# Performance work log

Measured on AMD Instinct MI355X. Metric: run time of the kernel, lower is better.

## Reference

```python
import jax, jax.numpy as jnp
import numpy as np


def _gcn_norm(edge_index, num_nodes):
    # Add self-loops (PyG SGConv default add_self_loops=True) and compute
    # symmetric normalization deg^-1/2 * A_hat * deg^-1/2.
    src, dst = edge_index[0], edge_index[1]
    loop = jnp.arange(num_nodes, dtype=src.dtype)
    src = jnp.concatenate([src, loop])
    dst = jnp.concatenate([dst, loop])
    ones = jnp.ones(src.shape[0], dtype=jnp.float32)
    deg = jax.ops.segment_sum(ones, dst, num_segments=num_nodes)
    dis = jnp.where(deg > 0, jax.lax.rsqrt(deg), 0.0)
    norm = dis[src] * dis[dst]  # per-edge weight
    return src, dst, norm


def _propagate(h, src, dst, norm, num_nodes, K):
    # K rounds of normalized sparse propagation: h <- A_hat_norm @ h
    for _ in range(K):
        h = jax.ops.segment_sum(h[src] * norm[:, None], dst, num_segments=num_nodes)
    return h


def setup_inputs() -> dict:
    key = jax.random.key(0)
    k1, k2, k3, k4 = jax.random.split(key, 4)
    N, E, F, H, C = 100000, 1600000, 128, 64, 40
    x = jax.random.normal(k1, (N, F), dtype=jnp.float32)
    edge_index = jax.random.randint(k2, (2, E), 0, N, dtype=jnp.int64)
    W1 = jax.random.normal(k3, (F, H), dtype=jnp.float32) * (1.0 / np.sqrt(F))
    b1 = jnp.zeros((H,), dtype=jnp.float32)
    W2 = jax.random.normal(k4, (H, C), dtype=jnp.float32) * (1.0 / np.sqrt(H))
    b2 = jnp.zeros((C,), dtype=jnp.float32)
    return {"x": x, "edge_index": edge_index, "W1": W1, "b1": b1, "W2": W2, "b2": b2}


def reference(x, edge_index, W1, b1, W2, b2):
    N = x.shape[0]
    K = 2
    src, dst, norm = _gcn_norm(edge_index, N)
    # SGConv layer 1: K-hop propagation then linear
    h = _propagate(x, src, dst, norm, N, K)
    h = h @ W1 + b1
    h = jax.nn.relu(h)
    # SGConv layer 2
    h = _propagate(h, src, dst, norm, N, K)
    h = h @ W2 + b2
    return jax.nn.log_softmax(h, axis=1)
```

## Files before the change

kernel.cpp:

```cpp
#include <hip/hip_runtime.h>
#include <hip/hip_fp16.h>
#include <math.h>

__host__ __device__ static inline int div_up(long long a, long long b) { return (int)((a + b - 1) / b); }

#define SCH 2048
#define PM 256
#define BKN 256
#define CAP 8192
#define PROPG 2048

struct h8 { __half2 a, b, c, d; };
struct h4 { __half2 a, b; };

typedef _Float16 half8v __attribute__((ext_vector_type(8)));
typedef float f32x4v __attribute__((ext_vector_type(4)));

__device__ inline int nt_load1(const int* p) {
    return __builtin_nontemporal_load(p);
}
__device__ inline h4 f4toh4(float4 v) {
    h4 o;
    o.a = __float22half2_rn(make_float2(v.x, v.y));
    o.b = __float22half2_rn(make_float2(v.z, v.w));
    return o;
}


__global__ __launch_bounds__(256) void k_histA(const int* __restrict__ dst,
                                               int* __restrict__ histA,
                                               int E, int NBK) {
    __shared__ int h[1024];
    const int tid = threadIdx.x, c = blockIdx.x;
    for (int i = tid; i < NBK; i += 256) h[i] = 0;
    __syncthreads();
    const int ce = (div_up(E, PM) + 3) & ~3;
    const int e0 = c * ce, e1 = min(E, e0 + ce);
    int i = e0 + tid * 4;
    for (; i + 3 < e1; i += 256 * 4) {
        int4 d = *reinterpret_cast<const int4*>(dst + i);
        atomicAdd(&h[d.x >> 8], 1);
        atomicAdd(&h[d.y >> 8], 1);
        atomicAdd(&h[d.z >> 8], 1);
        atomicAdd(&h[d.w >> 8], 1);
    }
    for (int j = i; j < e1; ++j) atomicAdd(&h[dst[j] >> 8], 1);
    __syncthreads();
    for (int b = tid; b < NBK; b += 256) histA[b * PM + c] = h[b];
}

__global__ void k_scan_part(const int* __restrict__ a, int* __restrict__ bsum, int len) {
    __shared__ int ws[4];
    int base = blockIdx.x * SCH + threadIdx.x * 8;
    int t = 0;
#pragma unroll
    for (int j = 0; j < 8; ++j) {
        int idx = base + j;
        if (idx < len) t += a[idx];
    }
    for (int off = 32; off >= 1; off >>= 1) t += __shfl_xor(t, off);
    int lane = threadIdx.x & 63, wid = threadIdx.x >> 6;
    if (lane == 0) ws[wid] = t;
    __syncthreads();
    if (threadIdx.x == 0) bsum[blockIdx.x] = ws[0] + ws[1] + ws[2] + ws[3];
}

__global__ void k_scan_bsums(int* __restrict__ bsum, int* __restrict__ tot, int NB) {
    __shared__ int wsum[16];
    int tid = threadIdx.x;
    int v = (tid < NB) ? bsum[tid] : 0;
    int lane = tid & 63, wid = tid >> 6;
    int x = v;
    for (int off = 1; off < 64; off <<= 1) {
        int y = __shfl_up(x, off);
        if (lane >= off) x += y;
    }
    if (lane == 63) wsum[wid] = x;
    __syncthreads();
    if (tid < 16) {
        int s = wsum[tid];
        for (int off = 1; off < 16; off <<= 1) {
            int y = __shfl_up(s, off);
            if (tid >= off) s += y;
        }
        wsum[tid] = s;
    }
    __syncthreads();
    int woff = (wid > 0) ? wsum[wid - 1] : 0;
    int excl = woff + x - v;
    if (tid < NB) bsum[tid] = excl;
    if (tid == NB - 1) tot[0] = excl + v;
}

__global__ void k_scan_apply(const int* __restrict__ cnt, const int* __restrict__ bsum,
                             int* __restrict__ rp, int* __restrict__ cur,
                             float* __restrict__ dis, float* __restrict__ inv, int N) {
    __shared__ int wsum[4];
    int tid = threadIdx.x;
    int base = blockIdx.x * SCH + tid * 8;
    int v[8];
    int t = 0;
#pragma unroll
    for (int j = 0; j < 8; ++j) {
        int idx = base + j;
        v[j] = (idx < N) ? cnt[idx] : 0;
        t += v[j];
    }
    int lane = tid & 63, wid = tid >> 6;
    int x = t;
    for (int off = 1; off < 64; off <<= 1) {
        int y = __shfl_up(x, off);
        if (lane >= off) x += y;
    }
    if (lane == 63) wsum[wid] = x;
    __syncthreads();
    int woff = 0;
    for (int w = 0; w < wid; ++w) woff += wsum[w];
    int run = bsum[blockIdx.x] + woff + (x - t);
#pragma unroll
    for (int j = 0; j < 8; ++j) {
        int idx = base + j;
        if (idx < N) {
            rp[idx] = run;
            cur[idx] = run;
            float dg = (float)v[j] + 1.0f;
            dis[idx] = rsqrtf(dg);
            inv[idx] = sqrtf(dg);
        }
        run += v[j];
    }
}

__global__ void k_scan_apply_plain(int* __restrict__ a, const int* __restrict__ bsum,
                                   int len) {
    __shared__ int wsum[4];
    int tid = threadIdx.x;
    int base = blockIdx.x * SCH + tid * 8;
    int v[8];
    int t = 0;
#pragma unroll
    for (int j = 0; j < 8; ++j) {
        int idx = base + j;
        v[j] = (idx < len) ? a[idx] : 0;
        t += v[j];
    }
    int lane = tid & 63, wid = tid >> 6;
    int x = t;
    for (int off = 1; off < 64; off <<= 1) {
        int y = __shfl_up(x, off);
        if (lane >= off) x += y;
    }
    if (lane == 63) wsum[wid] = x;
    __syncthreads();
    int woff = 0;
    for (int w = 0; w < wid; ++w) woff += wsum[w];
    int run = bsum[blockIdx.x] + woff + (x - t);
#pragma unroll
    for (int j = 0; j < 8; ++j) {
        int idx = base + j;
        if (idx < len) a[idx] = run;
        run += v[j];
    }
}

__global__ __launch_bounds__(256) void k_partitionA(
        const int* __restrict__ src, const int* __restrict__ dst,
        const int* __restrict__ pbase, unsigned* __restrict__ pairs, int E, int NBK) {
    __shared__ int curb[1024];
    const int tid = threadIdx.x, c = blockIdx.x;
    for (int b = tid; b < NBK; b += 256) curb[b] = pbase[b * PM + c];
    __syncthreads();
    const int ce = (div_up(E, PM) + 3) & ~3;
    const int e0 = c * ce, e1 = min(E, e0 + ce);
    int i = e0 + tid * 4;
    for (; i + 3 < e1; i += 256 * 4) {
        int4 d4 = *reinterpret_cast<const int4*>(dst + i);
        int4 s4 = *reinterpret_cast<const int4*>(src + i);
        int p0 = atomicAdd(&curb[d4.x >> 8], 1); pairs[p0] = ((unsigned)s4.x << 8) | (d4.x & 255);
        int p1 = atomicAdd(&curb[d4.y >> 8], 1); pairs[p1] = ((unsigned)s4.y << 8) | (d4.y & 255);
        int p2 = atomicAdd(&curb[d4.z >> 8], 1); pairs[p2] = ((unsigned)s4.z << 8) | (d4.z & 255);
        int p3 = atomicAdd(&curb[d4.w >> 8], 1); pairs[p3] = ((unsigned)s4.w << 8) | (d4.w & 255);
    }
    for (int j = i; j < e1; ++j) {
        int d = dst[j];
        int p = atomicAdd(&curb[d >> 8], 1);
        pairs[p] = ((unsigned)src[j] << 8) | (d & 255);
    }
}

__global__ __launch_bounds__(256) void k_cntB(
        const unsigned* __restrict__ pairs, const int* __restrict__ pbase,
        int* __restrict__ cnt, int E, int N, int NBK) {
    __shared__ int c256[BKN];
    const int b = blockIdx.x;
    const int tid = threadIdx.x;
    c256[tid] = 0;
    __syncthreads();
    const int base = pbase[b * PM];
    const int end = (b + 1 < NBK) ? pbase[(b + 1) * PM] : E;
    for (int i = base + tid; i < end; i += 256)
        atomicAdd(&c256[pairs[i] & 255], 1);
    __syncthreads();
    int n = b * BKN + tid;
    if (n < N) cnt[n] = c256[tid];
}

__global__ __launch_bounds__(256) void k_placeB(
        const unsigned* __restrict__ pairs, const int* __restrict__ rp,
        int* __restrict__ cur, int* __restrict__ csrc, int N) {
    __shared__ int curl[BKN];
    __shared__ int stage[CAP];
    const int b = blockIdx.x;
    const int n0 = b * BKN;
    const int n1 = min(N, n0 + BKN);
    const int base = rp[n0], end = rp[n1];
    const int cntb = end - base;
    const int tid = threadIdx.x;
    if (cntb <= CAP) {
        if (n0 + tid < n1) curl[tid] = rp[n0 + tid] - base;
        __syncthreads();
        for (int i = base + tid; i < end; i += 256) {
            unsigned pr = pairs[i];
            int p = atomicAdd(&curl[pr & 255], 1);
            stage[p] = (int)(pr >> 8);
        }
        __syncthreads();
        for (int i = tid; i < cntb; i += 256) csrc[base + i] = stage[i];
    } else {
        for (int i = base + tid; i < end; i += 256) {
            unsigned pr = pairs[i];
            int d = n0 + (int)(pr & 255);
            csrc[atomicAdd(&cur[d], 1)] = (int)(pr >> 8);
        }
    }
}


__device__ inline void add_h8(float* acc, const h8& v) {
    float2 f0 = __half22float2(v.a), f1 = __half22float2(v.b);
    float2 f2 = __half22float2(v.c), f3 = __half22float2(v.d);
    acc[0] += f0.x; acc[1] += f0.y;
    acc[2] += f1.x; acc[3] += f1.y;
    acc[4] += f2.x; acc[5] += f2.y;
    acc[6] += f3.x; acc[7] += f3.y;
}

template<int F>
__global__ __launch_bounds__(256) void k_prop_h(
        const int* __restrict__ rp, const int* __restrict__ csrc,
        const float* __restrict__ dis,
        const __half* __restrict__ hin, __half* __restrict__ hout, int N) {
    constexpr int TPE = F / 8;
    const long long total = (long long)N * TPE;
    const long long stride = (long long)gridDim.x * 256;
    for (long long t = (long long)blockIdx.x * 256 + threadIdx.x; t < total; t += stride) {
        int n = (int)(t / TPE);
        int l = (int)(t % TPE);
        float acc[8];
        {
            h8 v = *reinterpret_cast<const h8*>(hin + (size_t)n * F + 8 * l);
#pragma unroll
            for (int j = 0; j < 8; ++j) acc[j] = 0.f;
            add_h8(acc, v);
        }
        int e = rp[n], end = rp[n + 1];
        for (; e + 7 < end; e += 8) {
            int s[8];
            h8 v[8];
#pragma unroll
            for (int j = 0; j < 8; ++j) s[j] = nt_load1(csrc + e + j);
#pragma unroll
            for (int j = 0; j < 8; ++j)
                v[j] = *reinterpret_cast<const h8*>(hin + (size_t)s[j] * F + 8 * l);
#pragma unroll
            for (int j = 0; j < 8; ++j) add_h8(acc, v[j]);
        }
        for (; e < end; ++e) {
            int s = nt_load1(csrc + e);
            h8 v = *reinterpret_cast<const h8*>(hin + (size_t)s * F + 8 * l);
            add_h8(acc, v);
        }
        float dn = dis[n];
        float d2 = dn * dn;
        h8 o;
        o.a = __float22half2_rn(make_float2(acc[0] * d2, acc[1] * d2));
        o.b = __float22half2_rn(make_float2(acc[2] * d2, acc[3] * d2));
        o.c = __float22half2_rn(make_float2(acc[4] * d2, acc[5] * d2));
        o.d = __float22half2_rn(make_float2(acc[6] * d2, acc[7] * d2));
        *reinterpret_cast<h8*>(hout + (size_t)n * F + 8 * l) = o;
    }
}


__global__ __launch_bounds__(256) void k_gemm1(const float* __restrict__ X,
                                               const float* __restrict__ W,
                                               const float* __restrict__ dis,
                                               __half* __restrict__ Y, int N) {
    __shared__ __half sx[64][136];
    const int tid = threadIdx.x;
    const int lane = tid & 63, wv = tid >> 6;
    const int n0 = blockIdx.x * 64;
    const bool full = (n0 + 64 <= N);
    const int krow = (lane >> 4) * 8;
    const int col = lane & 15;

    half8v bfrag[4][4];
#pragma unroll
    for (int ct = 0; ct < 4; ++ct)
#pragma unroll
        for (int ks = 0; ks < 4; ++ks)
#pragma unroll
            for (int j = 0; j < 8; ++j)
                bfrag[ct][ks][j] = (_Float16)W[(ks * 32 + krow + j) * 64 + ct * 16 + col];

    float4 xr[8];
#pragma unroll
    for (int j = 0; j < 8; ++j) {
        int idx = (tid + j * 256) * 4;
        int n = idx >> 7, k = idx & 127;
        float4 v = make_float4(0.f, 0.f, 0.f, 0.f);
        if (full || n0 + n < N)
            v = *reinterpret_cast<const float4*>(X + (size_t)(n0 + n) * 128 + k);
        xr[j] = v;
    }
#pragma unroll
    for (int j = 0; j < 8; ++j) {
        int idx = (tid + j * 256) * 4;
        int n = idx >> 7, k = idx & 127;
        *reinterpret_cast<h4*>(&sx[n][k]) = f4toh4(xr[j]);
    }
    __syncthreads();

    const int m0 = wv * 16;
    f32x4v acc[4] = {{0,0,0,0},{0,0,0,0},{0,0,0,0},{0,0,0,0}};
#pragma unroll
    for (int ks = 0; ks < 4; ++ks) {
        half8v a = *reinterpret_cast<const half8v*>(&sx[m0 + (lane & 15)][ks * 32 + krow]);
#pragma unroll
        for (int ct = 0; ct < 4; ++ct)
            acc[ct] = __builtin_amdgcn_mfma_f32_16x16x32_f16(a, bfrag[ct][ks], acc[ct], 0, 0, 0);
    }

    const int rbase = m0 + (lane >> 4) * 4;
#pragma unroll
    for (int r = 0; r < 4; ++r) {
        int n = n0 + rbase + r;
        if (n < N) {
            float sc = dis[n];
#pragma unroll
            for (int ct = 0; ct < 4; ++ct)
                Y[(size_t)n * 64 + ct * 16 + col] = (__half)(acc[ct][r] * sc);
        }
    }
}

__global__ __launch_bounds__(256) void k_gemm2(const __half* __restrict__ H,
                                               const float* __restrict__ b1,
                                               const float* __restrict__ W2,
                                               const float* __restrict__ dis,
                                               const float* __restrict__ inv,
                                               __half* __restrict__ T, int N) {
    __shared__ float sh[64][68];
    __shared__ float sw[64][68];
    const int tid = threadIdx.x;
    const int n0 = blockIdx.x * 64;
    const bool full = (n0 + 64 <= N);
#pragma unroll
    for (int j = 0; j < 4; ++j) {
        int idx = (tid + j * 256) * 4;
        int k = idx >> 6, h = idx & 63;
        float4 v = make_float4(0.f, 0.f, 0.f, 0.f);
        if (h < 40) v = *reinterpret_cast<const float4*>(W2 + k * 40 + h);
        *reinterpret_cast<float4*>(&sw[k][h]) = v;
    }
#pragma unroll
    for (int j = 0; j < 2; ++j) {
        int idx = (tid + j * 256) * 8;
        int n = idx >> 6, k = idx & 63;
        float v[8];
        if (full || n0 + n < N) {
            float iv = inv[n0 + n];
            h8 hv = *reinterpret_cast<const h8*>(H + (size_t)(n0 + n) * 64 + k);
            float2 f0 = __half22float2(hv.a), f1 = __half22float2(hv.b);
            float2 f2 = __half22float2(hv.c), f3 = __half22float2(hv.d);
            v[0] = f0.x; v[1] = f0.y; v[2] = f1.x; v[3] = f1.y;
            v[4] = f2.x; v[5] = f2.y; v[6] = f3.x; v[7] = f3.y;
#pragma unroll
            for (int q = 0; q < 8; ++q) v[q] = fmaxf(v[q] * iv + b1[k + q], 0.f);
        } else {
#pragma unroll
            for (int q = 0; q < 8; ++q) v[q] = 0.f;
        }
#pragma unroll
        for (int q = 0; q < 8; ++q) sh[n][k + q] = v[q];
    }
    __syncthreads();
    const int lane = tid & 63, wid = tid >> 6;
    const int h0 = (lane & 15) * 4;
    const int nb = wid * 16 + (lane >> 4) * 4;
    float4 a0 = {0,0,0,0}, a1 = {0,0,0,0}, a2 = {0,0,0,0}, a3 = {0,0,0,0};
#define FMA4(a, s, v) { (a).x += (s) * (v).x; (a).y += (s) * (v).y; \
                        (a).z += (s) * (v).z; (a).w += (s) * (v).w; }
#pragma unroll 4
    for (int k0 = 0; k0 < 64; k0 += 4) {
        float4 x0 = *reinterpret_cast<float4*>(&sh[nb + 0][k0]);
        float4 x1 = *reinterpret_cast<float4*>(&sh[nb + 1][k0]);
        float4 x2 = *reinterpret_cast<float4*>(&sh[nb + 2][k0]);
        float4 x3 = *reinterpret_cast<float4*>(&sh[nb + 3][k0]);
        float4 w0 = *reinterpret_cast<float4*>(&sw[k0 + 0][h0]);
        float4 w1 = *reinterpret_cast<float4*>(&sw[k0 + 1][h0]);
        float4 w2 = *reinterpret_cast<float4*>(&sw[k0 + 2][h0]);
        float4 w3 = *reinterpret_cast<float4*>(&sw[k0 + 3][h0]);
        FMA4(a0, x0.x, w0); FMA4(a0, x0.y, w1); FMA4(a0, x0.z, w2); FMA4(a0, x0.w, w3);
        FMA4(a1, x1.x, w0); FMA4(a1, x1.y, w1); FMA4(a1, x1.z, w2); FMA4(a1, x1.w, w3);
        FMA4(a2, x2.x, w0); FMA4(a2, x2.y, w1); FMA4(a2, x2.z, w2); FMA4(a2, x2.w, w3);
        FMA4(a3, x3.x, w0); FMA4(a3, x3.y, w1); FMA4(a3, x3.z, w2); FMA4(a3, x3.w, w3);
    }
    if (h0 < 40) {
        int n = n0 + nb;
#pragma unroll
        for (int r = 0; r < 4; ++r) {
            float4 a = (r == 0) ? a0 : (r == 1) ? a1 : (r == 2) ? a2 : a3;
            if (n + r < N) {
                float sc = dis[n + r];
                h4 o;
                o.a = __float22half2_rn(make_float2(a.x * sc, a.y * sc));
                o.b = __float22half2_rn(make_float2(a.z * sc, a.w * sc));
                *reinterpret_cast<h4*>(T + (size_t)(n + r) * 40 + h0) = o;
            }
        }
    }
}

__global__ void k_bias_lsm(const __half* __restrict__ T, const float* __restrict__ b2,
                           const float* __restrict__ inv, float* __restrict__ Y, int N) {
    int gid = blockIdx.x * blockDim.x + threadIdx.x;
    int node = gid >> 6;
    int lane = threadIdx.x & 63;
    if (node >= N) return;
    float iv = inv[node];
    float v = (lane < 40) ? __half2float(T[(size_t)node * 40 + lane]) * iv + b2[lane]
                          : -INFINITY;
    float m = v;
    for (int off = 32; off >= 1; off >>= 1) m = fmaxf(m, __shfl_xor(m, off));
    float ev = (lane < 40) ? expf(v - m) : 0.0f;
    float s = ev;
    for (int off = 32; off >= 1; off >>= 1) s += __shfl_xor(s, off);
    if (lane < 40) Y[(size_t)node * 40 + lane] = v - m - logf(s);
}


extern "C" void kernel_launch(void* const* d_in, const int* in_sizes, int n_in,
                              void* d_out, int out_size, void* d_ws, size_t ws_size,
                              hipStream_t stream) {
    const float* x  = (const float*)d_in[0];
    const int*   ei = (const int*)d_in[1];
    const float* W1 = (const float*)d_in[2];
    const float* b1 = (const float*)d_in[3];
    const float* W2 = (const float*)d_in[4];
    const float* b2 = (const float*)d_in[5];
    float* out = (float*)d_out;

    const int H = in_sizes[3];
    const int F = in_sizes[2] / H;
    const int N = in_sizes[0] / F;
    const int E = in_sizes[1] / 2;
    (void)ws_size; (void)n_in; (void)out_size;

    const int* src = ei;
    const int* dst = ei + E;
    const int NSB = div_up(N, SCH);
    const int NBK = div_up(N, BKN);
    const int lenA = NBK * PM;
    const int NSA = div_up(lenA, SCH);

    const int Npad = (N + 256) & ~255;
    float* dis   = (float*)d_ws;
    float* inv   = dis + Npad;
    int*   cnt   = (int*)(inv + Npad);
    int*   rp    = cnt + Npad;
    int*   cur   = rp + Npad;
    int*   bsum  = cur + Npad;
    int*   bsumA = bsum + 256;
    int*   histA = bsumA + 256;
    int*   csrc  = histA + ((lenA + 255) & ~255);
    __half* bufA = (__half*)(csrc + ((E + 255) & ~255));
    __half* bufB = bufA + (size_t)N * 64;
    unsigned* pairs = (unsigned*)bufB;

    const int B = 256;

    k_histA<<<PM, 256, 0, stream>>>(dst, histA, E, NBK);
    k_scan_part<<<NSA, 256, 0, stream>>>(histA, bsumA, lenA);
    k_scan_bsums<<<1, 1024, 0, stream>>>(bsumA, bsumA + 128, NSA);
    k_scan_apply_plain<<<NSA, 256, 0, stream>>>(histA, bsumA, lenA);
    k_partitionA<<<PM, 256, 0, stream>>>(src, dst, histA, pairs, E, NBK);
    k_cntB<<<NBK, 256, 0, stream>>>(pairs, histA, cnt, E, N, NBK);
    k_scan_part<<<NSB, 256, 0, stream>>>(cnt, bsum, N);
    k_scan_bsums<<<1, 1024, 0, stream>>>(bsum, rp + N, NSB);
    k_scan_apply<<<NSB, 256, 0, stream>>>(cnt, bsum, rp, cur, dis, inv, N);
    k_placeB<<<NBK, 256, 0, stream>>>(pairs, rp, cur, csrc, N);

    k_gemm1<<<div_up(N, 64), 256, 0, stream>>>(x, W1, dis, bufA, N);
    k_prop_h<64><<<PROPG, B, 0, stream>>>(rp, csrc, dis, bufA, bufB, N);
    k_prop_h<64><<<PROPG, B, 0, stream>>>(rp, csrc, dis, bufB, bufA, N);

    k_gemm2<<<div_up(N, 64), 256, 0, stream>>>(bufA, b1, W2, dis, inv, bufB, N);
    k_prop_h<40><<<PROPG, B, 0, stream>>>(rp, csrc, dis, bufB, bufA, N);
    k_prop_h<40><<<PROPG, B, 0, stream>>>(rp, csrc, dis, bufA, bufB, N);

    k_bias_lsm<<<div_up((long long)N * 64, 256), 256, 0, stream>>>(bufB, b2, inv, out, N);
}
```

Before: 271.1 us.

## Fuse bucket count, scan and placement into one kernel; use MFMA for gemm2

Merges the per-bucket count kernel, the global node-degree scan (three kernels) and the placement kernel into a single k_placeB2. Each bucket's base offset is already known from the bucket-level scan, so row pointers come from a block-local scan, and the cnt, cur and bsum buffers are dropped. Separately, gemm2 is rewritten to keep H in fp16 shared memory and use 16x16x32 f16 MFMA with W2 fragments held in registers, replacing the scalar fp32 FMA loop. This removes four launches and a pass over pairs. The cost is that the pairs array is read twice inside one kernel and W2 is rounded to fp16.

```diff
diff --git a/kernel.cpp b/kernel.cpp
--- a/kernel.cpp
+++ b/kernel.cpp
@@ -90,45 +90,6 @@
     int excl = woff + x - v;
     if (tid < NB) bsum[tid] = excl;
     if (tid == NB - 1) tot[0] = excl + v;
-}
-
-__global__ void k_scan_apply(const int* __restrict__ cnt, const int* __restrict__ bsum,
-                             int* __restrict__ rp, int* __restrict__ cur,
-                             float* __restrict__ dis, float* __restrict__ inv, int N) {
-    __shared__ int wsum[4];
-    int tid = threadIdx.x;
-    int base = blockIdx.x * SCH + tid * 8;
-    int v[8];
-    int t = 0;
-#pragma unroll
-    for (int j = 0; j < 8; ++j) {
-        int idx = base + j;
-        v[j] = (idx < N) ? cnt[idx] : 0;
-        t += v[j];
-    }
-    int lane = tid & 63, wid = tid >> 6;
-    int x = t;
-    for (int off = 1; off < 64; off <<= 1) {
-        int y = __shfl_up(x, off);
-        if (lane >= off) x += y;
-    }
-    if (lane == 63) wsum[wid] = x;
-    __syncthreads();
-    int woff = 0;
-    for (int w = 0; w < wid; ++w) woff += wsum[w];
-    int run = bsum[blockIdx.x] + woff + (x - t);
-#pragma unroll
-    for (int j = 0; j < 8; ++j) {
-        int idx = base + j;
-        if (idx < N) {
-            rp[idx] = run;
-            cur[idx] = run;
-            float dg = (float)v[j] + 1.0f;
-            dis[idx] = rsqrtf(dg);
-            inv[idx] = sqrtf(dg);
-        }
-        run += v[j];
-    }
 }
 
 __global__ void k_scan_apply_plain(int* __restrict__ a, const int* __restrict__ bsum,
@@ -188,40 +149,51 @@
     }
 }
 
-__global__ __launch_bounds__(256) void k_cntB(
+__global__ __launch_bounds__(256) void k_placeB2(
         const unsigned* __restrict__ pairs, const int* __restrict__ pbase,
-        int* __restrict__ cnt, int E, int N, int NBK) {
-    __shared__ int c256[BKN];
+        int* __restrict__ rp, float* __restrict__ dis, float* __restrict__ inv,
+        int* __restrict__ csrc, int E, int N, int NBK) {
+    __shared__ int cnt256[BKN];
+    __shared__ int wsum[4];
+    __shared__ int stage[CAP];
     const int b = blockIdx.x;
     const int tid = threadIdx.x;
-    c256[tid] = 0;
-    __syncthreads();
+    const int n0 = b * BKN;
     const int base = pbase[b * PM];
     const int end = (b + 1 < NBK) ? pbase[(b + 1) * PM] : E;
+    const int cntb = end - base;
+    cnt256[tid] = 0;
+    __syncthreads();
     for (int i = base + tid; i < end; i += 256)
-        atomicAdd(&c256[pairs[i] & 255], 1);
-    __syncthreads();
-    int n = b * BKN + tid;
-    if (n < N) cnt[n] = c256[tid];
-}
-
-__global__ __launch_bounds__(256) void k_placeB(
-        const unsigned* __restrict__ pairs, const int* __restrict__ rp,
-        int* __restrict__ cur, int* __restrict__ csrc, int N) {
-    __shared__ int curl[BKN];
-    __shared__ int stage[CAP];
-    const int b = blockIdx.x;
-    const int n0 = b * BKN;
-    const int n1 = min(N, n0 + BKN);
-    const int base = rp[n0], end = rp[n1];
-    const int cntb = end - base;
-    const int tid = threadIdx.x;
+        atomicAdd(&cnt256[pairs[i] & 255], 1);
+    __syncthreads();
+    const int v = cnt256[tid];
+    const int lane = tid & 63, wid = tid >> 6;
+    int x = v;
+    for (int off = 1; off < 64; off <<= 1) {
+        int y = __shfl_up(x, off);
+        if (lane >= off) x += y;
+    }
+    if (lane == 63) wsum[wid] = x;
+    __syncthreads();
+    int woff = 0;
+    for (int w = 0; w < wid; ++w) woff += wsum[w];
+    const int ex = woff + x - v;
+    const int n = n0 + tid;
+    if (n < N) {
+        rp[n] = base + ex;
+        float dg = (float)v + 1.0f;
+        dis[n] = rsqrtf(dg);
+        inv[n] = sqrtf(dg);
+    }
+    if (b == NBK - 1 && tid == 255) rp[N] = base + ex + v;
+    __syncthreads();
+    cnt256[tid] = ex;
+    __syncthreads();
     if (cntb <= CAP) {
-        if (n0 + tid < n1) curl[tid] = rp[n0 + tid] - base;
-        __syncthreads();
         for (int i = base + tid; i < end; i += 256) {
             unsigned pr = pairs[i];
-            int p = atomicAdd(&curl[pr & 255], 1);
+            int p = atomicAdd(&cnt256[pr & 255], 1);
             stage[p] = (int)(pr >> 8);
         }
         __syncthreads();
@@ -229,8 +201,8 @@
     } else {
         for (int i = base + tid; i < end; i += 256) {
             unsigned pr = pairs[i];
-            int d = n0 + (int)(pr & 255);
-            csrc[atomicAdd(&cur[d], 1)] = (int)(pr >> 8);
+            int p = atomicAdd(&cnt256[pr & 255], 1);
+            csrc[base + p] = (int)(pr >> 8);
         }
     }
 }
@@ -360,19 +332,26 @@
                                                const float* __restrict__ dis,
                                                const float* __restrict__ inv,
                                                __half* __restrict__ T, int N) {
-    __shared__ float sh[64][68];
-    __shared__ float sw[64][68];
+    __shared__ __half sh[64][72];
     const int tid = threadIdx.x;
+    const int lane = tid & 63, wv = tid >> 6;
     const int n0 = blockIdx.x * 64;
     const bool full = (n0 + 64 <= N);
-#pragma unroll
-    for (int j = 0; j < 4; ++j) {
-        int idx = (tid + j * 256) * 4;
-        int k = idx >> 6, h = idx & 63;
-        float4 v = make_float4(0.f, 0.f, 0.f, 0.f);
-        if (h < 40) v = *reinterpret_cast<const float4*>(W2 + k * 40 + h);
-        *reinterpret_cast<float4*>(&sw[k][h]) = v;
-    }
+    const int krow = (lane >> 4) * 8;
+    const int col = lane & 15;
+
+    half8v bfrag[3][2];
+#pragma unroll
+    for (int ct = 0; ct < 3; ++ct)
+#pragma unroll
+        for (int ks = 0; ks < 2; ++ks)
+#pragma unroll
+            for (int j = 0; j < 8; ++j) {
+                int c = ct * 16 + col;
+                bfrag[ct][ks][j] = (c < 40) ? (_Float16)W2[(ks * 32 + krow + j) * 40 + c]
+                                            : (_Float16)0.f;
+            }
+
 #pragma unroll
     for (int j = 0; j < 2; ++j) {
         int idx = (tid + j * 256) * 8;
@@ -391,42 +370,35 @@
 #pragma unroll
             for (int q = 0; q < 8; ++q) v[q] = 0.f;
         }
-#pragma unroll
-        for (int q = 0; q < 8; ++q) sh[n][k + q] = v[q];
-    }
-    __syncthreads();
-    const int lane = tid & 63, wid = tid >> 6;
-    const int h0 = (lane & 15) * 4;
-    const int nb = wid * 16 + (lane >> 4) * 4;
-    float4 a0 = {0,0,0,0}, a1 = {0,0,0,0}, a2 = {0,0,0,0}, a3 = {0,0,0,0};
-#define FMA4(a, s, v) { (a).x += (s) * (v).x; (a).y += (s) * (v).y; \
-                        (a).z += (s) * (v).z; (a).w += (s) * (v).w; }
-#pragma unroll 4
-    for (int k0 = 0; k0 < 64; k0 += 4) {
-        float4 x0 = *reinterpret_cast<float4*>(&sh[nb + 0][k0]);
-        float4 x1 = *reinterpret_cast<float4*>(&sh[nb + 1][k0]);
-        float4 x2 = *reinterpret_cast<float4*>(&sh[nb + 2][k0]);
-        float4 x3 = *reinterpret_cast<float4*>(&sh[nb + 3][k0]);
-        float4 w0 = *reinterpret_cast<float4*>(&sw[k0 + 0][h0]);
-        float4 w1 = *reinterpret_cast<float4*>(&sw[k0 + 1][h0]);
-        float4 w2 = *reinterpret_cast<float4*>(&sw[k0 + 2][h0]);
-        float4 w3 = *reinterpret_cast<float4*>(&sw[k0 + 3][h0]);
-        FMA4(a0, x0.x, w0); FMA4(a0, x0.y, w1); FMA4(a0, x0.z, w2); FMA4(a0, x0.w, w3);
-        FMA4(a1, x1.x, w0); FMA4(a1, x1.y, w1); FMA4(a1, x1.z, w2); FMA4(a1, x1.w, w3);
-        FMA4(a2, x2.x, w0); FMA4(a2, x2.y, w1); FMA4(a2, x2.z, w2); FMA4(a2, x2.w, w3);
-        FMA4(a3, x3.x, w0); FMA4(a3, x3.y, w1); FMA4(a3, x3.z, w2); FMA4(a3, x3.w, w3);
-    }
-    if (h0 < 40) {
-        int n = n0 + nb;
-#pragma unroll
-        for (int r = 0; r < 4; ++r) {
-            float4 a = (r == 0) ? a0 : (r == 1) ? a1 : (r == 2) ? a2 : a3;
-            if (n + r < N) {
-                float sc = dis[n + r];
-                h4 o;
-                o.a = __float22half2_rn(make_float2(a.x * sc, a.y * sc));
-                o.b = __float22half2_rn(make_float2(a.z * sc, a.w * sc));
-                *reinterpret_cast<h4*>(T + (size_t)(n + r) * 40 + h0) = o;
+        h8 o;
+        o.a = __float22half2_rn(make_float2(v[0], v[1]));
+        o.b = __float22half2_rn(make_float2(v[2], v[3]));
+        o.c = __float22half2_rn(make_float2(v[4], v[5]));
+        o.d = __float22half2_rn(make_float2(v[6], v[7]));
+        *reinterpret_cast<h8*>(&sh[n][k]) = o;
+    }
+    __syncthreads();
+
+    const int m0 = wv * 16;
+    f32x4v acc[3] = {{0,0,0,0},{0,0,0,0},{0,0,0,0}};
+#pragma unroll
+    for (int ks = 0; ks < 2; ++ks) {
+        half8v a = *reinterpret_cast<const half8v*>(&sh[m0 + (lane & 15)][ks * 32 + krow]);
+#pragma unroll
+        for (int ct = 0; ct < 3; ++ct)
+            acc[ct] = __builtin_amdgcn_mfma_f32_16x16x32_f16(a, bfrag[ct][ks], acc[ct], 0, 0, 0);
+    }
+
+    const int rbase = m0 + (lane >> 4) * 4;
+#pragma unroll
+    for (int r = 0; r < 4; ++r) {
+        int n = n0 + rbase + r;
+        if (n < N) {
+            float sc = dis[n];
+#pragma unroll
+            for (int ct = 0; ct < 3; ++ct) {
+                int c = ct * 16 + col;
+                if (c < 40) T[(size_t)n * 40 + c] = (__half)(acc[ct][r] * sc);
             }
         }
     }
@@ -469,7 +441,6 @@
 
     const int* src = ei;
     const int* dst = ei + E;
-    const int NSB = div_up(N, SCH);
     const int NBK = div_up(N, BKN);
     const int lenA = NBK * PM;
     const int NSA = div_up(lenA, SCH);
@@ -477,11 +448,8 @@
     const int Npad = (N + 256) & ~255;
     float* dis   = (float*)d_ws;
     float* inv   = dis + Npad;
-    int*   cnt   = (int*)(inv + Npad);
-    int*   rp    = cnt + Npad;
-    int*   cur   = rp + Npad;
-    int*   bsum  = cur + Npad;
-    int*   bsumA = bsum + 256;
+    int*   rp    = (int*)(inv + Npad);
+    int*   bsumA = rp + Npad;
     int*   histA = bsumA + 256;
     int*   csrc  = histA + ((lenA + 255) & ~255);
     __half* bufA = (__half*)(csrc + ((E + 255) & ~255));
@@ -495,11 +463,7 @@
     k_scan_bsums<<<1, 1024, 0, stream>>>(bsumA, bsumA + 128, NSA);
     k_scan_apply_plain<<<NSA, 256, 0, stream>>>(histA, bsumA, lenA);
     k_partitionA<<<PM, 256, 0, stream>>>(src, dst, histA, pairs, E, NBK);
-    k_cntB<<<NBK, 256, 0, stream>>>(pairs, histA, cnt, E, N, NBK);
-    k_scan_part<<<NSB, 256, 0, stream>>>(cnt, bsum, N);
-    k_scan_bsums<<<1, 1024, 0, stream>>>(bsum, rp + N, NSB);
-    k_scan_apply<<<NSB, 256, 0, stream>>>(cnt, bsum, rp, cur, dis, inv, N);
-    k_placeB<<<NBK, 256, 0, stream>>>(pairs, rp, cur, csrc, N);
+    k_placeB2<<<NBK, 256, 0, stream>>>(pairs, histA, rp, dis, inv, csrc, E, N, NBK);
 
     k_gemm1<<<div_up(N, 64), 256, 0, stream>>>(x, W1, dis, bufA, N);
     k_prop_h<64><<<PROPG, B, 0, stream>>>(rp, csrc, dis, bufA, bufB, N);
```

New measurement: 252.4 us. -6.9%, faster.
